# Kernel tuning notes

Hardware: AMD Instinct MI355X
Metric: run time of the kernel (lower is better)

## Reference

```python
import jax, jax.numpy as jnp
import numpy as np

N = 102400      # total nodes
E = 1638400     # total edges (avg degree 16)
B = 2048        # number of graphs
DIN = 128       # input feature dim
K = 30          # sort-pool k


def setup_inputs() -> dict:
    key = jax.random.key(0)
    ks = jax.random.split(key, 16)
    x = jax.random.normal(ks[0], (N, DIN), dtype=jnp.float32)
    edge_index = jax.random.randint(ks[1], (2, E), 0, N)
    batch = jnp.sort(jax.random.randint(ks[2], (N,), 0, B))

    def w(k, sh):
        return jax.random.normal(k, sh, dtype=jnp.float32) * 0.1

    return {
        "x": x, "edge_index": edge_index, "batch": batch,
        "W1": w(ks[3], (DIN, 32)), "b1": w(ks[4], (32,)),
        "W2": w(ks[5], (32, 32)), "b2": w(ks[6], (32,)),
        "W3": w(ks[7], (32, 32)), "b3": w(ks[8], (32,)),
        "W4": w(ks[9], (32, 1)), "b4": w(ks[10], (1,)),
        "conv1_w": w(ks[11], (16, 1, 97)), "conv1_b": w(ks[11], (16,)),
        "conv2_w": w(ks[12], (32, 16, 5)), "conv2_b": w(ks[12], (32,)),
        "lin1_w": w(ks[13], (352, 128)), "lin1_b": w(ks[13], (128,)),
        "lin2_w": w(ks[14], (128, 1)), "lin2_b": w(ks[14], (1,)),
    }


def _gcn(x, W, b, src, dst, dinv, n):
    # PyG GCNConv: D^{-1/2}(A+I)D^{-1/2} X W + b, transform first (small out dim)
    h = x @ W
    msg = h[src] * (dinv[src] * dinv[dst])[:, None]            # [E, F]
    agg = jax.ops.segment_sum(msg, dst, num_segments=n)        # neighbor aggregation
    agg = agg + h * (dinv * dinv)[:, None]                     # self-loop term (norm = 1/deg)
    return agg + b


def _sort_pool(h, batch, num_graphs, k):
    # global_sort_pool: per-graph descending sort by last channel, keep top-k, zero-pad
    n, f = h.shape
    order = jnp.lexsort((-h[:, -1], batch))                    # primary: graph id, secondary: -key
    hs, bs = h[order], batch[order]
    counts = jax.ops.segment_sum(jnp.ones(n, jnp.int32), batch, num_segments=num_graphs)
    starts = jnp.cumsum(counts) - counts                       # exclusive prefix
    pos = jnp.arange(n) - starts[bs]                           # rank within graph
    keep = pos < k
    out = jnp.zeros((num_graphs, k, f), h.dtype)
    out = out.at[bs, jnp.clip(pos, 0, k - 1)].add(jnp.where(keep[:, None], hs, 0.0))
    return out.reshape(num_graphs, k * f)


def _conv1d(x, w, b, stride):
    y = jax.lax.conv_general_dilated(x, w, (stride,), 'VALID',
                                     dimension_numbers=('NCH', 'OIH', 'NCH'))
    return y + b[None, :, None]


def reference(x, edge_index, batch, W1, b1, W2, b2, W3, b3, W4, b4,
              conv1_w, conv1_b, conv2_w, conv2_b, lin1_w, lin1_b, lin2_w, lin2_b):
    n = x.shape[0]
    src, dst = edge_index[0], edge_index[1]
    deg = jax.ops.segment_sum(jnp.ones(src.shape[0], x.dtype), dst, num_segments=n) + 1.0
    dinv = jax.lax.rsqrt(deg)

    h1 = jnp.tanh(_gcn(x, W1, b1, src, dst, dinv, n))
    h2 = jnp.tanh(_gcn(h1, W2, b2, src, dst, dinv, n))
    h3 = jnp.tanh(_gcn(h2, W3, b3, src, dst, dinv, n))
    h4 = jnp.tanh(_gcn(h3, W4, b4, src, dst, dinv, n))
    h = jnp.concatenate([h1, h2, h3, h4], axis=-1)             # [N, 97]

    h = _sort_pool(h, batch, B, K)                             # [B, 2910]
    h = h[:, None, :]                                          # [B, 1, 2910]
    h = jax.nn.relu(_conv1d(h, conv1_w, conv1_b, 97))          # [B, 16, 30]
    bsz, c, l = h.shape
    h = h.reshape(bsz, c, l // 2, 2).max(axis=-1)              # maxpool(2,2) -> [B,16,15]
    h = jax.nn.relu(_conv1d(h, conv2_w, conv2_b, 1))           # [B, 32, 11]
    h = h.reshape(bsz, -1)                                     # [B, 352]
    h = jax.nn.relu(h @ lin1_w + lin1_b)
    # Dropout(0.5) is identity at inference
    return jax.nn.sigmoid(h @ lin2_w + lin2_b)                 # [B, 1]
```

## Files before the change

### kernel.cpp

```cpp
#include <hip/hip_runtime.h>
#include <math.h>

#define NN 102400
#define NE 1638400
#define NG 2048
#define KTOP 30
#define NBUCK 400
#define EPB 4096
#define NB1 400

__global__ __launch_bounds__(256) void fused_front_kernel(
    const int* __restrict__ dst, int* __restrict__ hist1,
    const float* __restrict__ x, const float* __restrict__ W1,
    float* __restrict__ htmp,
    const int* __restrict__ batch, int* __restrict__ starts) {
    __shared__ float Wsh[128 * 32];
    __shared__ int hsh[NBUCK];
    int bid = blockIdx.x;
    int tid = threadIdx.x;

    if (bid < NB1) {
        for (int q = tid; q < NBUCK; q += 256) hsh[q] = 0;
        __syncthreads();
        const int4* dp = (const int4*)(dst + bid * EPB);
        for (int i4 = tid; i4 < EPB / 4; i4 += 256) {
            int4 dd = dp[i4];
            atomicAdd(&hsh[dd.x >> 8], 1);
            atomicAdd(&hsh[dd.y >> 8], 1);
            atomicAdd(&hsh[dd.z >> 8], 1);
            atomicAdd(&hsh[dd.w >> 8], 1);
        }
        __syncthreads();
        for (int q = tid; q < NBUCK; q += 256) hist1[q * NB1 + bid] = hsh[q];
    } else if (bid < NB1 + 800) {
        int bidx = bid - NB1;
        for (int i = tid; i < 128 * 32; i += 256) Wsh[i] = W1[i];
        __syncthreads();
        int jb = (tid >> 6) << 3;
        int q = tid & 63;
        int n0 = bidx * 128 + q;
        int n1 = n0 + 64;
        const float* x0p = x + (size_t)n0 * 128;
        const float* x1p = x + (size_t)n1 * 128;
        float acc0[8], acc1[8];
#pragma unroll
        for (int j = 0; j < 8; ++j) { acc0[j] = 0.f; acc1[j] = 0.f; }
#pragma unroll 2
        for (int k = 0; k < 128; k += 4) {
            float4 xa = *(const float4*)(x0p + k);
            float4 xb = *(const float4*)(x1p + k);
            float xs0[4] = {xa.x, xa.y, xa.z, xa.w};
            float xs1[4] = {xb.x, xb.y, xb.z, xb.w};
#pragma unroll
            for (int kk = 0; kk < 4; ++kk) {
                float4 wlo = *(const float4*)&Wsh[(k + kk) * 32 + jb];
                float4 whi = *(const float4*)&Wsh[(k + kk) * 32 + jb + 4];
                float v0 = xs0[kk], v1 = xs1[kk];
                acc0[0] += v0 * wlo.x; acc0[1] += v0 * wlo.y;
                acc0[2] += v0 * wlo.z; acc0[3] += v0 * wlo.w;
                acc0[4] += v0 * whi.x; acc0[5] += v0 * whi.y;
                acc0[6] += v0 * whi.z; acc0[7] += v0 * whi.w;
                acc1[0] += v1 * wlo.x; acc1[1] += v1 * wlo.y;
                acc1[2] += v1 * wlo.z; acc1[3] += v1 * wlo.w;
                acc1[4] += v1 * whi.x; acc1[5] += v1 * whi.y;
                acc1[6] += v1 * whi.z; acc1[7] += v1 * whi.w;
            }
        }
        float4 o0 = {acc0[0], acc0[1], acc0[2], acc0[3]};
        float4 o1 = {acc0[4], acc0[5], acc0[6], acc0[7]};
        float4 o2 = {acc1[0], acc1[1], acc1[2], acc1[3]};
        float4 o3 = {acc1[4], acc1[5], acc1[6], acc1[7]};
        *(float4*)&htmp[(size_t)n0 * 32 + jb] = o0;
        *(float4*)&htmp[(size_t)n0 * 32 + jb + 4] = o1;
        *(float4*)&htmp[(size_t)n1 * 32 + jb] = o2;
        *(float4*)&htmp[(size_t)n1 * 32 + jb + 4] = o3;
    } else {
        int i = (bid - NB1 - 800) * 256 + tid;
        if (i < NN) {
            int c = batch[i];
            int p = (i == 0) ? -1 : batch[i - 1];
            for (int g = p + 1; g <= c; ++g) starts[g] = i;
            if (i == NN - 1) {
                for (int g = c + 1; g <= NG; ++g) starts[g] = NN;
            }
        }
    }
}

__global__ __launch_bounds__(256) void s1a_kernel(const int* __restrict__ hist1,
                                                  int* __restrict__ offs,
                                                  int* __restrict__ totals) {
    __shared__ int A[512], B[512];
    int q = blockIdx.x, tid = threadIdx.x;
    int i0 = tid, i1 = tid + 256;
    int v0 = (i0 < NB1) ? hist1[q * NB1 + i0] : 0;
    int v1 = (i1 < NB1) ? hist1[q * NB1 + i1] : 0;
    A[i0] = v0; A[i1] = v1;
    __syncthreads();
    int* cur = A; int* nxt = B;
    for (int off = 1; off < 512; off <<= 1) {
        nxt[i0] = cur[i0] + ((i0 >= off) ? cur[i0 - off] : 0);
        nxt[i1] = cur[i1] + cur[i1 - off];
        __syncthreads();
        int* t = cur; cur = nxt; nxt = t;
    }
    if (i0 < NB1) offs[q * NB1 + i0] = cur[i0] - v0;
    if (i1 < NB1) offs[q * NB1 + i1] = cur[i1] - v1;
    if (tid == 0) totals[q] = cur[511];
}

__global__ __launch_bounds__(256) void s1b_kernel(const int* __restrict__ totals,
                                                  int* __restrict__ bucketStart,
                                                  int* __restrict__ rowptr) {
    __shared__ int A[512], B[512];
    int tid = threadIdx.x;
    int i0 = tid, i1 = tid + 256;
    int v0 = (i0 < NBUCK) ? totals[i0] : 0;
    int v1 = (i1 < NBUCK) ? totals[i1] : 0;
    A[i0] = v0; A[i1] = v1;
    __syncthreads();
    int* cur = A; int* nxt = B;
    for (int off = 1; off < 512; off <<= 1) {
        nxt[i0] = cur[i0] + ((i0 >= off) ? cur[i0 - off] : 0);
        nxt[i1] = cur[i1] + cur[i1 - off];
        __syncthreads();
        int* t = cur; cur = nxt; nxt = t;
    }
    if (i0 < NBUCK) bucketStart[i0] = cur[i0] - v0;
    if (i1 < NBUCK) bucketStart[i1] = cur[i1] - v1;
    if (tid == 0) { bucketStart[NBUCK] = cur[511]; rowptr[NN] = cur[511]; }
}

__global__ __launch_bounds__(256) void p1_kernel(const int* __restrict__ src,
                                                 const int* __restrict__ dst,
                                                 const int* __restrict__ offs,
                                                 const int* __restrict__ bucketStart,
                                                 unsigned int* __restrict__ ebuf) {
    __shared__ int myoff[NBUCK];
    int b = blockIdx.x, tid = threadIdx.x;
    for (int q = tid; q < NBUCK; q += 256)
        myoff[q] = bucketStart[q] + offs[q * NB1 + b];
    __syncthreads();
    const int4* dp = (const int4*)(dst + b * EPB);
    const int4* sp = (const int4*)(src + b * EPB);
    for (int i4 = tid; i4 < EPB / 4; i4 += 256) {
        int4 dd = dp[i4];
        int4 ss = sp[i4];
        int p0 = atomicAdd(&myoff[dd.x >> 8], 1);
        int p1 = atomicAdd(&myoff[dd.y >> 8], 1);
        int p2 = atomicAdd(&myoff[dd.z >> 8], 1);
        int p3 = atomicAdd(&myoff[dd.w >> 8], 1);
        ebuf[p0] = ((unsigned int)(dd.x & 255) << 24) | (unsigned int)ss.x;
        ebuf[p1] = ((unsigned int)(dd.y & 255) << 24) | (unsigned int)ss.y;
        ebuf[p2] = ((unsigned int)(dd.z & 255) << 24) | (unsigned int)ss.z;
        ebuf[p3] = ((unsigned int)(dd.w & 255) << 24) | (unsigned int)ss.w;
    }
}

__global__ __launch_bounds__(256) void p2_kernel(const unsigned int* __restrict__ ebuf,
                                                 const int* __restrict__ bucketStart,
                                                 int* __restrict__ csr_src,
                                                 int* __restrict__ rowptr,
                                                 float* __restrict__ dinv) {
    __shared__ int fcnt[256];
    __shared__ int tmp[256];
    __shared__ int foff[256];
    int q = blockIdx.x, tid = threadIdx.x;
    int base = bucketStart[q];
    int ecnt = bucketStart[q + 1] - base;
    fcnt[tid] = 0;
    __syncthreads();
    for (int i = tid; i < ecnt; i += 256) {
        unsigned int e = ebuf[base + i];
        atomicAdd(&fcnt[e >> 24], 1);
    }
    __syncthreads();
    int c = fcnt[tid];
    int n = q * 256 + tid;
    dinv[n] = rsqrtf((float)c + 1.0f);
    tmp[tid] = c;
    __syncthreads();
    for (int off = 1; off < 256; off <<= 1) {
        int u = (tid >= off) ? tmp[tid - off] : 0;
        __syncthreads();
        tmp[tid] += u;
        __syncthreads();
    }
    int excl = base + tmp[tid] - c;
    rowptr[n] = excl;
    foff[tid] = excl;
    __syncthreads();
    for (int i = tid; i < ecnt; i += 256) {
        unsigned int e = ebuf[base + i];
        int pos = atomicAdd(&foff[e >> 24], 1);
        csr_src[pos] = (int)(e & 0xFFFFFF);
    }
}

template <int NEXT>
__global__ __launch_bounds__(256) void gcn_aggd_kernel(
    const int* __restrict__ rowptr, const int* __restrict__ csr_src,
    const float* __restrict__ htmp, const float* __restrict__ dinv,
    const float* __restrict__ b, const float* __restrict__ Wn,
    float* __restrict__ hout, float* __restrict__ htn) {
    __shared__ float Ws[32 * 32];
    __shared__ float Hs[32][36];
    int tid = threadIdx.x;
    if (NEXT == 32) {
        for (int i = tid; i < 1024; i += 256) Ws[i] = Wn[i];
    } else {
        if (tid < 32) Ws[tid] = Wn[tid];
    }
    int idx = blockIdx.x * 256 + tid;
    int n = idx >> 3, fg = (idx & 7) << 2;
    int beg = rowptr[n], end = rowptr[n + 1];
    float di = dinv[n];
    float4 acc = {0.f, 0.f, 0.f, 0.f};
    int i = beg;
    for (; i + 7 < end; i += 8) {
        int s[8];
#pragma unroll
        for (int k = 0; k < 8; ++k) s[k] = csr_src[i + k];
        float c[8];
#pragma unroll
        for (int k = 0; k < 8; ++k) c[k] = dinv[s[k]] * di;
        float4 v[8];
#pragma unroll
        for (int k = 0; k < 8; ++k) v[k] = *(const float4*)&htmp[(size_t)s[k] * 32 + fg];
#pragma unroll
        for (int k = 0; k < 8; ++k) {
            acc.x += v[k].x * c[k]; acc.y += v[k].y * c[k];
            acc.z += v[k].z * c[k]; acc.w += v[k].w * c[k];
        }
    }
    for (; i + 3 < end; i += 4) {
        int s0 = csr_src[i], s1 = csr_src[i + 1];
        int s2 = csr_src[i + 2], s3 = csr_src[i + 3];
        float c0 = dinv[s0] * di, c1 = dinv[s1] * di;
        float c2 = dinv[s2] * di, c3 = dinv[s3] * di;
        float4 v0 = *(const float4*)&htmp[(size_t)s0 * 32 + fg];
        float4 v1 = *(const float4*)&htmp[(size_t)s1 * 32 + fg];
        float4 v2 = *(const float4*)&htmp[(size_t)s2 * 32 + fg];
        float4 v3 = *(const float4*)&htmp[(size_t)s3 * 32 + fg];
        acc.x += v0.x * c0; acc.y += v0.y * c0; acc.z += v0.z * c0; acc.w += v0.w * c0;
        acc.x += v1.x * c1; acc.y += v1.y * c1; acc.z += v1.z * c1; acc.w += v1.w * c1;
        acc.x += v2.x * c2; acc.y += v2.y * c2; acc.z += v2.z * c2; acc.w += v2.w * c2;
        acc.x += v3.x * c3; acc.y += v3.y * c3; acc.z += v3.z * c3; acc.w += v3.w * c3;
    }
    for (; i < end; ++i) {
        int s = csr_src[i];
        float c = dinv[s] * di;
        float4 v = *(const float4*)&htmp[(size_t)s * 32 + fg];
        acc.x += v.x * c; acc.y += v.y * c; acc.z += v.z * c; acc.w += v.w * c;
    }
    float dd = di * di;
    float4 hs = *(const float4*)&htmp[(size_t)n * 32 + fg];
    float4 bb = *(const float4*)&b[fg];
    float4 o;
    o.x = tanhf(acc.x + hs.x * dd + bb.x);
    o.y = tanhf(acc.y + hs.y * dd + bb.y);
    o.z = tanhf(acc.z + hs.z * dd + bb.z);
    o.w = tanhf(acc.w + hs.w * dd + bb.w);
    *(float4*)&hout[(size_t)n * 32 + fg] = o;
    int nl = tid >> 3;
    *(float4*)&Hs[nl][fg] = o;
    __syncthreads();
    if (NEXT == 32) {
        int n2 = tid >> 3, j4 = (tid & 7) << 2;
        int gnode = blockIdx.x * 32 + n2;
        float4 r = {0.f, 0.f, 0.f, 0.f};
#pragma unroll
        for (int k = 0; k < 32; ++k) {
            float h = Hs[n2][k];
            float4 wv = *(const float4*)&Ws[k * 32 + j4];
            r.x += h * wv.x; r.y += h * wv.y; r.z += h * wv.z; r.w += h * wv.w;
        }
        *(float4*)&htn[(size_t)gnode * 32 + j4] = r;
    } else {
        if (tid < 32) {
            int gnode = blockIdx.x * 32 + tid;
            float s = 0.f;
#pragma unroll
            for (int k = 0; k < 32; ++k) s += Hs[tid][k] * Ws[k];
            htn[gnode] = s;
        }
    }
}

__global__ __launch_bounds__(256) void gcn_agg1_kernel(
    const int* __restrict__ rowptr, const int* __restrict__ csr_src,
    const float* __restrict__ htmp, const float* __restrict__ dinv,
    const float* __restrict__ b, float* __restrict__ hout) {
    int n = blockIdx.x * blockDim.x + threadIdx.x;
    if (n >= NN) return;
    int beg = rowptr[n], end = rowptr[n + 1];
    float di = dinv[n];
    float acc = 0.f;
    int i = beg;
    for (; i + 7 < end; i += 8) {
        int s[8];
#pragma unroll
        for (int k = 0; k < 8; ++k) s[k] = csr_src[i + k];
        float c[8], v[8];
#pragma unroll
        for (int k = 0; k < 8; ++k) c[k] = dinv[s[k]] * di;
#pragma unroll
        for (int k = 0; k < 8; ++k) v[k] = htmp[s[k]];
#pragma unroll
        for (int k = 0; k < 8; ++k) acc += v[k] * c[k];
    }
    for (; i < end; ++i) {
        int s = csr_src[i];
        acc += htmp[s] * (dinv[s] * di);
    }
    hout[n] = tanhf(acc + htmp[n] * di * di + b[0]);
}


#define PSTR 96

__global__ __launch_bounds__(256) void pool_cnn_kernel(
    const float* __restrict__ h1, const float* __restrict__ h2,
    const float* __restrict__ h3, const float* __restrict__ h4,
    const int* __restrict__ starts,
    const float* __restrict__ c1w, const float* __restrict__ c1b,
    const float* __restrict__ c2w, const float* __restrict__ c2b,
    const float* __restrict__ l1w, const float* __restrict__ l1b,
    const float* __restrict__ l2w, const float* __restrict__ l2b,
    float* __restrict__ out) {
    __shared__ float P[KTOP][PSTR];
    __shared__ float pkey[KTOP];
    __shared__ float CW[16 * 97];
    __shared__ float KY[480];
    __shared__ int   sel_node[KTOP];
    __shared__ float sel_key[KTOP];
    float* keys = KY;
    float* y2 = &P[0][0];
    float* y3 = &P[0][0] + 240;
    float* z  = &P[0][0] + 592;
    int g = blockIdx.x;
    int tid = threadIdx.x;

    int start = starts[g];
    int end = starts[g + 1];
    int cnt = end - start;

    for (int i = tid; i < KTOP * PSTR; i += 256) (&P[0][0])[i] = 0.f;
    if (tid < KTOP) pkey[tid] = 0.f;
    for (int i = tid; i < 16 * 97; i += 256) CW[i] = c1w[i];
    bool fits = (cnt <= 480);
    if (fits) {
        for (int i = tid; i < cnt; i += 256) keys[i] = h4[start + i];
    }
    __syncthreads();

    for (int i = tid; i < cnt; i += 256) {
        float key = fits ? keys[i] : h4[start + i];
        int rank = 0;
        if (fits) {
            for (int j = 0; j < cnt; ++j) {
                float kj = keys[j];
                rank += (kj > key) || (kj == key && j < i);
            }
        } else {
            for (int j = 0; j < cnt; ++j) {
                float kj = h4[start + j];
                rank += (kj > key) || (kj == key && j < i);
            }
        }
        if (rank < KTOP) {
            sel_node[rank] = start + i;
            sel_key[rank] = key;
        }
    }
    __syncthreads();

    int nsel = (cnt < KTOP) ? cnt : KTOP;
    for (int u = tid; u < nsel * 24; u += 256) {
        int r = u / 24, q = u % 24;
        int node = sel_node[r];
        const float* srcp = (q < 8) ? h1 : (q < 16) ? h2 : h3;
        int qq = q & 7;
        float4 v = *(const float4*)(srcp + (size_t)node * 32 + 4 * qq);
        *(float4*)&P[r][(q < 8 ? 0 : (q < 16 ? 32 : 64)) + 4 * qq] = v;
    }
    for (int r = tid; r < nsel; r += 256) pkey[r] = sel_key[r];
    __syncthreads();

    for (int o = tid; o < 16 * KTOP; o += 256) {
        int t = o >> 4, c = o & 15;
        float s = c1b[c];
        const float* Pr = &P[t][0];
        const float* Wr = &CW[c * 97];
#pragma unroll
        for (int f4 = 0; f4 < 24; ++f4) {
            float4 pv = *(const float4*)(Pr + 4 * f4);
            s += Wr[4 * f4 + 0] * pv.x;
            s += Wr[4 * f4 + 1] * pv.y;
            s += Wr[4 * f4 + 2] * pv.z;
            s += Wr[4 * f4 + 3] * pv.w;
        }
        s += Wr[96] * pkey[t];
        KY[c * KTOP + t] = fmaxf(s, 0.f);
    }
    __syncthreads();

    for (int o = tid; o < 16 * 15; o += 256) {
        int c = o / 15, t = o % 15;
        y2[o] = fmaxf(KY[c * KTOP + 2 * t], KY[c * KTOP + 2 * t + 1]);
    }
    __syncthreads();

    for (int o = tid; o < 32 * 11; o += 256) {
        int c = o / 11, t = o % 11;
        float s = c2b[c];
#pragma unroll
        for (int i = 0; i < 16; ++i)
#pragma unroll
            for (int j = 0; j < 5; ++j)
                s += c2w[(c * 16 + i) * 5 + j] * y2[i * 15 + t + j];
        y3[o] = fmaxf(s, 0.f);
    }
    __syncthreads();

    for (int o = tid; o < 128; o += 256) {
        float s = l1b[o];
#pragma unroll 16
        for (int i = 0; i < 352; ++i) s += y3[i] * l1w[i * 128 + o];
        z[o] = fmaxf(s, 0.f);
    }
    __syncthreads();

    if (tid == 0) {
        float s = l2b[0];
#pragma unroll 4
        for (int i = 0; i < 128; ++i) s += z[i] * l2w[i];
        out[g] = 1.f / (1.f + expf(-s));
    }
}

extern "C" void kernel_launch(void* const* d_in, const int* in_sizes, int n_in,
                              void* d_out, int out_size, void* d_ws, size_t ws_size,
                              hipStream_t stream) {
    const float* x   = (const float*)d_in[0];
    const int* ei    = (const int*)d_in[1];
    const int* batch = (const int*)d_in[2];
    const float* W1  = (const float*)d_in[3];
    const float* b1  = (const float*)d_in[4];
    const float* W2  = (const float*)d_in[5];
    const float* b2  = (const float*)d_in[6];
    const float* W3  = (const float*)d_in[7];
    const float* b3  = (const float*)d_in[8];
    const float* W4  = (const float*)d_in[9];
    const float* b4  = (const float*)d_in[10];
    const float* c1w = (const float*)d_in[11];
    const float* c1b = (const float*)d_in[12];
    const float* c2w = (const float*)d_in[13];
    const float* c2b = (const float*)d_in[14];
    const float* l1w = (const float*)d_in[15];
    const float* l1b = (const float*)d_in[16];
    const float* l2w = (const float*)d_in[17];
    const float* l2b = (const float*)d_in[18];
    float* out = (float*)d_out;

    const int* srcp = ei;
    const int* dstp = ei + NE;

    char* w = (char*)d_ws;
    float* dinv      = (float*)w;               w += sizeof(float) * NN;
    float* htmpA     = (float*)w;               w += sizeof(float) * NN * 32;
    float* htmpB     = (float*)w;               w += sizeof(float) * NN * 32;
    float* h1        = (float*)w;               w += sizeof(float) * NN * 32;
    float* h2        = (float*)w;               w += sizeof(float) * NN * 32;
    float* h3        = (float*)w;               w += sizeof(float) * NN * 32;
    float* h4        = (float*)w;               w += sizeof(float) * NN;
    int*   rowptr    = (int*)w;                 w += sizeof(int) * (NN + 1);
    int*   hist1     = (int*)w;                 w += sizeof(int) * NBUCK * NB1;
    int*   offs      = (int*)w;                 w += sizeof(int) * NBUCK * NB1;
    int*   totals    = (int*)w;                 w += sizeof(int) * NBUCK;
    int*   bucketStart = (int*)w;               w += sizeof(int) * (NBUCK + 1);
    int*   csr_src   = (int*)w;                 w += sizeof(int) * NE;
    int*   starts    = (int*)w;                 w += sizeof(int) * (NG + 1);

    unsigned int* ebuf = (unsigned int*)h2;

    fused_front_kernel<<<NB1 + 800 + 400, 256, 0, stream>>>(dstp, hist1, x, W1, htmpA,
                                                            batch, starts);
    s1a_kernel<<<NBUCK, 256, 0, stream>>>(hist1, offs, totals);
    s1b_kernel<<<1, 256, 0, stream>>>(totals, bucketStart, rowptr);
    p1_kernel<<<NB1, 256, 0, stream>>>(srcp, dstp, offs, bucketStart, ebuf);
    p2_kernel<<<NBUCK, 256, 0, stream>>>(ebuf, bucketStart, csr_src, rowptr, dinv);

    gcn_aggd_kernel<32><<<NN / 32, 256, 0, stream>>>(rowptr, csr_src, htmpA, dinv, b1,
                                                     W2, h1, htmpB);
    gcn_aggd_kernel<32><<<NN / 32, 256, 0, stream>>>(rowptr, csr_src, htmpB, dinv, b2,
                                                     W3, h2, htmpA);
    gcn_aggd_kernel<1><<<NN / 32, 256, 0, stream>>>(rowptr, csr_src, htmpA, dinv, b3,
                                                    W4, h3, htmpB);
    gcn_agg1_kernel<<<NN / 256, 256, 0, stream>>>(rowptr, csr_src, htmpB, dinv, b4, h4);

    pool_cnn_kernel<<<NG, 256, 0, stream>>>(h1, h2, h3, h4, starts,
                                            c1w, c1b, c2w, c2b,
                                            l1w, l1b, l2w, l2b, out);
}
```

Before: 254.4 us.

## Split MLP head into batched kernel reusing lin1 weights across 16 graphs

The per-graph pool/CNN kernel now stops after conv2 and writes the 352-wide features to a workspace buffer. A new head kernel processes 16 graphs per block, so each lin1 weight load feeds 8 graphs per thread instead of being re-read by every graph block, and only 128 threads no longer sit idle during the linear layer. The sort key is also folded into padded row 96 of the pooled tile. The cost is an extra launch and a global round trip for the intermediate features.

Measured after the change: 256.2 us. Within noise of the previous version (+0.7%).

```diff
diff --git a/kernel.cpp b/kernel.cpp
--- a/kernel.cpp
+++ b/kernel.cpp
@@ -8,6 +8,7 @@
 #define NBUCK 400
 #define EPB 4096
 #define NB1 400
+#define GB 16
 
 __global__ __launch_bounds__(256) void fused_front_kernel(
     const int* __restrict__ dst, int* __restrict__ hist1,
@@ -317,27 +318,23 @@
 }
 
 
-#define PSTR 96
-
-__global__ __launch_bounds__(256) void pool_cnn_kernel(
+#define PSTR 100
+
+__global__ __launch_bounds__(256) void pool_conv_kernel(
     const float* __restrict__ h1, const float* __restrict__ h2,
     const float* __restrict__ h3, const float* __restrict__ h4,
     const int* __restrict__ starts,
     const float* __restrict__ c1w, const float* __restrict__ c1b,
     const float* __restrict__ c2w, const float* __restrict__ c2b,
-    const float* __restrict__ l1w, const float* __restrict__ l1b,
-    const float* __restrict__ l2w, const float* __restrict__ l2b,
-    float* __restrict__ out) {
+    float* __restrict__ y3g) {
     __shared__ float P[KTOP][PSTR];
-    __shared__ float pkey[KTOP];
     __shared__ float CW[16 * 97];
     __shared__ float KY[480];
+    __shared__ float sel_key[KTOP];
     __shared__ int   sel_node[KTOP];
-    __shared__ float sel_key[KTOP];
     float* keys = KY;
     float* y2 = &P[0][0];
     float* y3 = &P[0][0] + 240;
-    float* z  = &P[0][0] + 592;
     int g = blockIdx.x;
     int tid = threadIdx.x;
 
@@ -346,7 +343,6 @@
     int cnt = end - start;
 
     for (int i = tid; i < KTOP * PSTR; i += 256) (&P[0][0])[i] = 0.f;
-    if (tid < KTOP) pkey[tid] = 0.f;
     for (int i = tid; i < 16 * 97; i += 256) CW[i] = c1w[i];
     bool fits = (cnt <= 480);
     if (fits) {
@@ -384,7 +380,7 @@
         float4 v = *(const float4*)(srcp + (size_t)node * 32 + 4 * qq);
         *(float4*)&P[r][(q < 8 ? 0 : (q < 16 ? 32 : 64)) + 4 * qq] = v;
     }
-    for (int r = tid; r < nsel; r += 256) pkey[r] = sel_key[r];
+    for (int r = tid; r < nsel; r += 256) P[r][96] = sel_key[r];
     __syncthreads();
 
     for (int o = tid; o < 16 * KTOP; o += 256) {
@@ -400,7 +396,7 @@
             s += Wr[4 * f4 + 2] * pv.z;
             s += Wr[4 * f4 + 3] * pv.w;
         }
-        s += Wr[96] * pkey[t];
+        s += Wr[96] * Pr[96];
         KY[c * KTOP + t] = fmaxf(s, 0.f);
     }
     __syncthreads();
@@ -423,19 +419,40 @@
     }
     __syncthreads();
 
-    for (int o = tid; o < 128; o += 256) {
-        float s = l1b[o];
-#pragma unroll 16
-        for (int i = 0; i < 352; ++i) s += y3[i] * l1w[i * 128 + o];
-        z[o] = fmaxf(s, 0.f);
-    }
-    __syncthreads();
-
-    if (tid == 0) {
+    for (int o = tid; o < 352; o += 256) y3g[(size_t)g * 352 + o] = y3[o];
+}
+
+__global__ __launch_bounds__(256) void head_kernel(
+    const float* __restrict__ y3g, const float* __restrict__ l1w,
+    const float* __restrict__ l1b, const float* __restrict__ l2w,
+    const float* __restrict__ l2b, float* __restrict__ out) {
+    __shared__ float Y[GB][352];
+    __shared__ float Z[GB][129];
+    int tid = threadIdx.x;
+    int g0 = blockIdx.x * GB;
+    const float4* srcp = (const float4*)(y3g + (size_t)g0 * 352);
+    for (int u = tid; u < GB * 88; u += 256) ((float4*)&Y[0][0])[u] = srcp[u];
+    __syncthreads();
+    int o = tid & 127;
+    int gp = tid >> 7;
+    float lb = l1b[o];
+    float acc[8];
+#pragma unroll
+    for (int j = 0; j < 8; ++j) acc[j] = lb;
+#pragma unroll 4
+    for (int i = 0; i < 352; ++i) {
+        float wv = l1w[i * 128 + o];
+#pragma unroll
+        for (int j = 0; j < 8; ++j) acc[j] += Y[gp * 8 + j][i] * wv;
+    }
+#pragma unroll
+    for (int j = 0; j < 8; ++j) Z[gp * 8 + j][o] = fmaxf(acc[j], 0.f);
+    __syncthreads();
+    if (tid < GB) {
         float s = l2b[0];
 #pragma unroll 4
-        for (int i = 0; i < 128; ++i) s += z[i] * l2w[i];
-        out[g] = 1.f / (1.f + expf(-s));
+        for (int i = 0; i < 128; ++i) s += Z[tid][i] * l2w[i];
+        out[g0 + tid] = 1.f / (1.f + expf(-s));
     }
 }
 
@@ -483,6 +500,7 @@
     int*   starts    = (int*)w;                 w += sizeof(int) * (NG + 1);
 
     unsigned int* ebuf = (unsigned int*)h2;
+    float* y3g = htmpA;
 
     fused_front_kernel<<<NB1 + 800 + 400, 256, 0, stream>>>(dstp, hist1, x, W1, htmpA,
                                                             batch, starts);
@@ -499,7 +517,7 @@
                                                     W4, h3, htmpB);
     gcn_agg1_kernel<<<NN / 256, 256, 0, stream>>>(rowptr, csr_src, htmpB, dinv, b4, h4);
 
-    pool_cnn_kernel<<<NG, 256, 0, stream>>>(h1, h2, h3, h4, starts,
-                                            c1w, c1b, c2w, c2b,
-                                            l1w, l1b, l2w, l2b, out);
-}
+    pool_conv_kernel<<<NG, 256, 0, stream>>>(h1, h2, h3, h4, starts,
+                                             c1w, c1b, c2w, c2b, y3g);
+    head_kernel<<<NG / GB, 256, 0, stream>>>(y3g, l1w, l1b, l2w, l2b, out);
+}
```
